# Kernel optimization log

Measured on AMD Instinct MI355X. Metric: run time of the kernel, lower is better.

## Reference

```python
import jax, jax.numpy as jnp
import numpy as np

INPUT_DIM = 768
STATE_DIM = 128
LN_EPS = 1e-5
CLAMP = 10.0


def setup_inputs() -> dict:
    key = jax.random.key(0)
    ks = jax.random.split(key, 9)
    B, T, D, S = 128, 256, INPUT_DIM, STATE_DIM
    x = jax.random.normal(ks[0], (B, T, D), dtype=jnp.float32)
    A = jax.random.normal(ks[1], (S, S), dtype=jnp.float32) * 0.01
    # nn.Linear weights are [out_features, in_features]
    B_w = jax.random.normal(ks[2], (S, D), dtype=jnp.float32) * (1.0 / np.sqrt(D))
    C_w = jax.random.normal(ks[3], (D, S), dtype=jnp.float32) * (1.0 / np.sqrt(S))
    D_w = jax.random.normal(ks[4], (D, D), dtype=jnp.float32) * (1.0 / np.sqrt(D))
    gate_w = jax.random.normal(ks[5], (2, D), dtype=jnp.float32) * (1.0 / np.sqrt(D))
    gate_b = jnp.zeros((2,), dtype=jnp.float32)
    ln_gamma = jnp.ones((D,), dtype=jnp.float32)
    ln_beta = jnp.zeros((D,), dtype=jnp.float32)
    return {"x": x, "A": A, "B_w": B_w, "C_w": C_w, "D_w": D_w,
            "gate_w": gate_w, "gate_b": gate_b,
            "ln_gamma": ln_gamma, "ln_beta": ln_beta}


def reference(x, A, B_w, C_w, D_w, gate_w, gate_b, ln_gamma, ln_beta):
    B, T, D = x.shape
    S = A.shape[0]
    residual = x
    # Precompute input projection for all timesteps: [B, T, S]
    Bx = jnp.einsum('btd,sd->bts', x, B_w)

    def step(state, bx_t):
        # state: [B, S]; state @ A.T + B(x_t), clamped
        state = jnp.clip(state @ A.T + bx_t, -CLAMP, CLAMP)
        return state, state

    init = jnp.zeros((B, S), dtype=x.dtype)
    _, states = jax.lax.scan(step, init, jnp.swapaxes(Bx, 0, 1))  # [T, B, S]
    states = jnp.swapaxes(states, 0, 1)  # [B, T, S]

    # Output projection (vectorized over all timesteps)
    out = jnp.einsum('bts,ds->btd', states, C_w) + jnp.einsum('btd,ed->bte', x, D_w)

    # Gating mix with residual
    gate = jax.nn.softmax(jnp.einsum('btd,gd->btg', x, gate_w) + gate_b, axis=-1)
    out = gate[..., 0:1] * out + gate[..., 1:2] * residual

    # LayerNorm (dropout is identity in eval)
    mu = jnp.mean(out, axis=-1, keepdims=True)
    var = jnp.var(out, axis=-1, keepdims=True)
    out = (out - mu) * jax.lax.rsqrt(var + LN_EPS) * ln_gamma + ln_beta
    return out
```

## Files before the change

kernel.cpp:

```cpp
#include <hip/hip_runtime.h>
#include <hip/hip_bf16.h>
#include <stdint.h>

typedef __bf16 bf16;
typedef __bf16 bf16x4 __attribute__((ext_vector_type(4)));
typedef __bf16 bf16x8 __attribute__((ext_vector_type(8)));
typedef float  f32x4  __attribute__((ext_vector_type(4)));

static constexpr int BB = 128;
static constexpr int TT = 256;
static constexpr int DD = 768;
static constexpr int SS = 128;
static constexpr int MM = BB * TT;
static constexpr int KW1 = DD + SS;

__device__ __forceinline__ void gload16(const void* g, void* l) {
  __builtin_amdgcn_global_load_lds(
      (const __attribute__((address_space(1))) void*)(uintptr_t)g,
      (__attribute__((address_space(3))) void*)(uintptr_t)l, 16, 0, 0);
}

__global__ __launch_bounds__(256) void k0_convert(
    const float* __restrict__ B_w, const float* __restrict__ D_w,
    const float* __restrict__ C_w, bf16* __restrict__ W0, bf16* __restrict__ W1) {
  int i = blockIdx.x * 256 + threadIdx.x;
  if (i < SS * DD) {
    W0[i] = (bf16)B_w[i];
  } else {
    int j = i - SS * DD;
    int n = j / KW1;
    int k = j - n * KW1;
    float v = (k < DD) ? D_w[n * DD + k] : C_w[n * SS + (k - DD)];
    W1[j] = (bf16)v;
  }
}

__global__ __launch_bounds__(256) void k0x_gate(
    const float* __restrict__ x, bf16* __restrict__ xb,
    const float* __restrict__ gw, const float* __restrict__ gb,
    float* __restrict__ glog) {
  const int lane = threadIdx.x & 63;
  const int wv = threadIdx.x >> 6;
  const int r = blockIdx.x * 4 + wv;
  const float4* xr = (const float4*)(x + (size_t)r * DD);
  const float4* g0w = (const float4*)gw;
  const float4* g1w = (const float4*)(gw + DD);
  float d = 0.f;
  #pragma unroll
  for (int i = 0; i < 3; ++i) {
    int c = i * 64 + lane;
    float4 v = xr[c];
    float4 w0 = g0w[c], w1 = g1w[c];
    d += v.x * (w0.x - w1.x) + v.y * (w0.y - w1.y)
       + v.z * (w0.z - w1.z) + v.w * (w0.w - w1.w);
    bf16x4 h;
    h[0] = (bf16)v.x; h[1] = (bf16)v.y; h[2] = (bf16)v.z; h[3] = (bf16)v.w;
    *(bf16x4*)&xb[(size_t)r * DD + c * 4] = h;
  }
  #pragma unroll
  for (int off = 32; off > 0; off >>= 1) d += __shfl_xor(d, off);
  if (lane == 0) glog[r] = d + gb[0] - gb[1];
}

template <int TAG>
__global__ __launch_bounds__(256) void kg(
    const bf16* __restrict__ A1, const bf16* __restrict__ A2,
    const bf16* __restrict__ W, void* __restrict__ Cv,
    int kt1, int kt2, int lda1, int lda2, int ldb, int ldc, int mode) {
  __shared__ __align__(16) bf16 As[128 * 64];
  __shared__ __align__(16) bf16 Bs[128 * 64];

  const int tid = threadIdx.x;
  const int lane = tid & 63;
  const int wv = tid >> 6;
  const int wr = wv >> 1, wc = wv & 1;
  const int lr = lane & 15, lh = lane >> 4;
  const int bn0 = blockIdx.x * 128;
  const int bm0 = blockIdx.y * 128;

  const int l_row = lane >> 3;
  const int l_col = (lane & 7) * 8;

  f32x4 acc[4][4] = {};
  const int KT = kt1 + kt2;

  for (int kt = 0; kt < KT; ++kt) {
    __syncthreads();
    {
      const bf16* Ab; int lda;
      if (kt < kt1) { Ab = A1 + (size_t)bm0 * lda1 + kt * 64; lda = lda1; }
      else          { Ab = A2 + (size_t)bm0 * lda2 + (kt - kt1) * 64; lda = lda2; }
      #pragma unroll
      for (int it = 0; it < 4; ++it) {
        int c = wv * 4 + it;
        gload16(Ab + (size_t)(c * 8 + l_row) * lda + l_col, &As[c * 512]);
      }
    }
    {
      const bf16* Bb = W + (size_t)bn0 * ldb + kt * 64;
      #pragma unroll
      for (int it = 0; it < 4; ++it) {
        int c = wv * 4 + it;
        gload16(Bb + (size_t)(c * 8 + l_row) * ldb + l_col, &Bs[c * 512]);
      }
    }
    __syncthreads();
    #pragma unroll
    for (int kk = 0; kk < 2; ++kk) {
      bf16x8 af[4], bfr[4];
      #pragma unroll
      for (int f = 0; f < 4; ++f)
        af[f] = *(const bf16x8*)&As[(wr * 64 + f * 16 + lr) * 64 + kk * 32 + lh * 8];
      #pragma unroll
      for (int f = 0; f < 4; ++f)
        bfr[f] = *(const bf16x8*)&Bs[(wc * 64 + f * 16 + lr) * 64 + kk * 32 + lh * 8];
      #pragma unroll
      for (int fi = 0; fi < 4; ++fi)
        #pragma unroll
        for (int fj = 0; fj < 4; ++fj)
          acc[fi][fj] = __builtin_amdgcn_mfma_f32_16x16x32_bf16(
              af[fi], bfr[fj], acc[fi][fj], 0, 0, 0);
    }
  }
  #pragma unroll
  for (int fi = 0; fi < 4; ++fi)
    #pragma unroll
    for (int fj = 0; fj < 4; ++fj) {
      int row = bm0 + wr * 64 + fi * 16 + lh * 4;
      int col = bn0 + wc * 64 + fj * 16 + lr;
      if (mode == 0) {
        float* Cp = (float*)Cv + (size_t)row * ldc + col;
        #pragma unroll
        for (int r = 0; r < 4; ++r) Cp[(size_t)r * ldc] = acc[fi][fj][r];
      } else if (mode == 1) {
        bf16* Cp = (bf16*)Cv + (size_t)row * ldc + col;
        #pragma unroll
        for (int r = 0; r < 4; ++r) Cp[(size_t)r * ldc] = (bf16)acc[fi][fj][r];
      } else {
        float* Cp = (float*)Cv + (size_t)row * ldc + col;
        #pragma unroll
        for (int r = 0; r < 4; ++r) Cp[(size_t)r * ldc] += acc[fi][fj][r];
      }
    }
}

__global__ __launch_bounds__(256) void k_fused(
    const bf16* __restrict__ xb, const bf16* __restrict__ W1,
    float* __restrict__ out, bf16* SB, const float* __restrict__ A) {
  __shared__ __align__(16) char sraw[34304];

  if (blockIdx.x < 128) {
    __builtin_amdgcn_s_setprio(1);
    float* st   = (float*)sraw;
    float* part = (float*)(sraw + 1024);
    float* bxb  = (float*)(sraw + 1536);

    const int tid = threadIdx.x;
    const int s = tid & 127;
    const int q = tid >> 7;
    bf16* Bxb = SB + (size_t)blockIdx.x * TT * SS;

    float areg[64];
    {
      const float* Ar = A + s * SS + q * 64;
      #pragma unroll
      for (int j = 0; j < 16; ++j) {
        float4 v = *(const float4*)(Ar + j * 4);
        areg[j * 4 + 0] = v.x; areg[j * 4 + 1] = v.y;
        areg[j * 4 + 2] = v.z; areg[j * 4 + 3] = v.w;
      }
    }
    if (tid < SS) st[tid] = 0.f;

    {
      bf16x8 c0 = *(const bf16x8*)(Bxb + tid * 16);
      bf16x8 c1 = *(const bf16x8*)(Bxb + tid * 16 + 8);
      float* d0 = &bxb[tid * 16];
      #pragma unroll
      for (int e = 0; e < 8; ++e) d0[e] = (float)c0[e];
      #pragma unroll
      for (int e = 0; e < 8; ++e) d0[8 + e] = (float)c1[e];
    }
    bf16x8 n0 = *(const bf16x8*)(Bxb + 4096 + tid * 16);
    bf16x8 n1 = *(const bf16x8*)(Bxb + 4096 + tid * 16 + 8);
    __syncthreads();

    int p = 0, cur = 0;
    for (int ch = 0; ch < 8; ++ch) {
      #pragma unroll 1
      for (int t2 = 0; t2 < 32; ++t2) {
        const float* stp = st + p * SS;
        float a0 = 0.f, a1 = 0.f, a2 = 0.f, a3 = 0.f;
        #pragma unroll
        for (int j = 0; j < 64; j += 4) {
          float4 sv = *(const float4*)(stp + (q << 6) + j);
          a0 += areg[j]     * sv.x;
          a1 += areg[j + 1] * sv.y;
          a2 += areg[j + 2] * sv.z;
          a3 += areg[j + 3] * sv.w;
        }
        float partial = (a0 + a1) + (a2 + a3);
        if (q) part[s] = partial;
        __syncthreads();
        if (!q) {
          float tot = partial + part[s] + bxb[cur * 4096 + t2 * SS + s];
          tot = fminf(10.f, fmaxf(-10.f, tot));
          st[(p ^ 1) * SS + s] = tot;
          Bxb[(size_t)(ch * 32 + t2) * SS + s] = (bf16)tot;
        }
        __syncthreads();
        p ^= 1;
      }
      if (ch < 7) {
        float* dn = &bxb[(cur ^ 1) * 4096 + tid * 16];
        #pragma unroll
        for (int e = 0; e < 8; ++e) dn[e] = (float)n0[e];
        #pragma unroll
        for (int e = 0; e < 8; ++e) dn[8 + e] = (float)n1[e];
        if (ch < 6) {
          n0 = *(const bf16x8*)(Bxb + (ch + 2) * 4096 + tid * 16);
          n1 = *(const bf16x8*)(Bxb + (ch + 2) * 4096 + tid * 16 + 8);
        }
        __syncthreads();
        cur ^= 1;
      }
    }
  } else {
    bf16* As = (bf16*)sraw;
    bf16* Bs = (bf16*)(sraw + 16384);

    const int gb = blockIdx.x - 128;
    const int bn0 = (gb % 6) * 128;
    const int bm0 = (gb / 6) * 128;

    const int tid = threadIdx.x;
    const int lane = tid & 63;
    const int wv = tid >> 6;
    const int wr = wv >> 1, wc = wv & 1;
    const int lr = lane & 15, lh = lane >> 4;
    const int l_row = lane >> 3;
    const int l_col = (lane & 7) * 8;

    f32x4 acc[4][4] = {};

    for (int kt = 0; kt < 12; ++kt) {
      __syncthreads();
      {
        const bf16* Ab = xb + (size_t)bm0 * DD + kt * 64;
        #pragma unroll
        for (int it = 0; it < 4; ++it) {
          int c = wv * 4 + it;
          gload16(Ab + (size_t)(c * 8 + l_row) * DD + l_col, &As[c * 512]);
        }
      }
      {
        const bf16* Bb = W1 + (size_t)bn0 * KW1 + kt * 64;
        #pragma unroll
        for (int it = 0; it < 4; ++it) {
          int c = wv * 4 + it;
          gload16(Bb + (size_t)(c * 8 + l_row) * KW1 + l_col, &Bs[c * 512]);
        }
      }
      __syncthreads();
      #pragma unroll
      for (int kk = 0; kk < 2; ++kk) {
        bf16x8 af[4], bfr[4];
        #pragma unroll
        for (int f = 0; f < 4; ++f)
          af[f] = *(const bf16x8*)&As[(wr * 64 + f * 16 + lr) * 64 + kk * 32 + lh * 8];
        #pragma unroll
        for (int f = 0; f < 4; ++f)
          bfr[f] = *(const bf16x8*)&Bs[(wc * 64 + f * 16 + lr) * 64 + kk * 32 + lh * 8];
        #pragma unroll
        for (int fi = 0; fi < 4; ++fi)
          #pragma unroll
          for (int fj = 0; fj < 4; ++fj)
            acc[fi][fj] = __builtin_amdgcn_mfma_f32_16x16x32_bf16(
                af[fi], bfr[fj], acc[fi][fj], 0, 0, 0);
      }
    }
    #pragma unroll
    for (int fi = 0; fi < 4; ++fi)
      #pragma unroll
      for (int fj = 0; fj < 4; ++fj) {
        int row = bm0 + wr * 64 + fi * 16 + lh * 4;
        int col = bn0 + wc * 64 + fj * 16 + lr;
        float* Cp = out + (size_t)row * DD + col;
        #pragma unroll
        for (int r = 0; r < 4; ++r) Cp[(size_t)r * DD] = acc[fi][fj][r];
      }
  }
}

__global__ __launch_bounds__(256) void kT(
    const bf16* __restrict__ SB, const bf16* __restrict__ Wc,
    float* __restrict__ out, const float* __restrict__ x,
    const float* __restrict__ glog, const float* __restrict__ ln_g,
    const float* __restrict__ ln_b) {
  __shared__ __align__(16) bf16 As[16 * 128];
  __shared__ __align__(16) bf16 Ws[128 * 128];
  __shared__ __align__(16) bf16 mbuf[16 * 768];
  __shared__ float wpart[4][16][2];
  __shared__ float mu_s[16], rs_s[16];

  const int tid = threadIdx.x;
  const int lane = tid & 63;
  const int wv = tid >> 6;
  const int lr = lane & 15, lh = lane >> 4;
  const int m0 = blockIdx.x * 16;

  {
    const bf16* g = SB + (size_t)(m0 + wv * 4 + lh) * 128 + lr * 8;
    gload16(g, &As[wv * 512]);
  }

  float g0v[4], g1v[4];
  #pragma unroll
  for (int r = 0; r < 4; ++r) {
    float gl = glog[m0 + lh * 4 + r];
    float g0 = 1.f / (1.f + expf(-gl));
    g0v[r] = g0; g1v[r] = 1.f - g0;
  }

  float s1[4] = {0.f, 0.f, 0.f, 0.f}, s2[4] = {0.f, 0.f, 0.f, 0.f};

  for (int st = 0; st < 6; ++st) {
    const int n0 = st * 128;
    __syncthreads();
    #pragma unroll
    for (int it = 0; it < 8; ++it) {
      int c = wv * 8 + it;
      const bf16* g = Wc + (size_t)(n0 + c * 4 + lh) * KW1 + lr * 8;
      gload16(g, &Ws[c * 512]);
    }
    __syncthreads();
    f32x4 acc0 = {0.f, 0.f, 0.f, 0.f}, acc1 = {0.f, 0.f, 0.f, 0.f};
    #pragma unroll
    for (int kk = 0; kk < 4; ++kk) {
      bf16x8 af = *(const bf16x8*)&As[lr * 128 + kk * 32 + lh * 8];
      bf16x8 b0 = *(const bf16x8*)&Ws[((wv * 2 + 0) * 16 + lr) * 128 + kk * 32 + lh * 8];
      bf16x8 b1 = *(const bf16x8*)&Ws[((wv * 2 + 1) * 16 + lr) * 128 + kk * 32 + lh * 8];
      acc0 = __builtin_amdgcn_mfma_f32_16x16x32_bf16(af, b0, acc0, 0, 0, 0);
      acc1 = __builtin_amdgcn_mfma_f32_16x16x32_bf16(af, b1, acc1, 0, 0, 0);
    }
    #pragma unroll
    for (int nn = 0; nn < 2; ++nn) {
      const f32x4 av = nn ? acc1 : acc0;
      int col = n0 + (wv * 2 + nn) * 16 + lr;
      #pragma unroll
      for (int r = 0; r < 4; ++r) {
        int rowl = lh * 4 + r;
        size_t gi = (size_t)(m0 + rowl) * DD + col;
        float raw = av[r] + out[gi];
        float mv = g0v[r] * raw + g1v[r] * x[gi];
        s1[r] += mv; s2[r] += mv * mv;
        mbuf[rowl * DD + col] = (bf16)mv;
      }
    }
  }
  #pragma unroll
  for (int r = 0; r < 4; ++r) {
    #pragma unroll
    for (int off = 1; off < 16; off <<= 1) {
      s1[r] += __shfl_xor(s1[r], off);
      s2[r] += __shfl_xor(s2[r], off);
    }
  }
  if (lr == 0) {
    #pragma unroll
    for (int r = 0; r < 4; ++r) {
      wpart[wv][lh * 4 + r][0] = s1[r];
      wpart[wv][lh * 4 + r][1] = s2[r];
    }
  }
  __syncthreads();
  if (tid < 16) {
    float S1 = wpart[0][tid][0] + wpart[1][tid][0] + wpart[2][tid][0] + wpart[3][tid][0];
    float S2 = wpart[0][tid][1] + wpart[1][tid][1] + wpart[2][tid][1] + wpart[3][tid][1];
    float mu = S1 * (1.f / 768.f);
    float var = S2 * (1.f / 768.f) - mu * mu;
    mu_s[tid] = mu;
    rs_s[tid] = rsqrtf(fmaxf(var, 0.f) + 1e-5f);
  }
  __syncthreads();
  #pragma unroll
  for (int i = 0; i < 12; ++i) {
    int gq = i * 256 + tid;
    int row = gq / 192;
    int c4 = gq - row * 192;
    int col = c4 * 4;
    bf16x4 mv = *(const bf16x4*)&mbuf[row * DD + col];
    float4 gg = *(const float4*)&ln_g[col];
    float4 bb = *(const float4*)&ln_b[col];
    float mu = mu_s[row], rs = rs_s[row];
    float4 y;
    y.x = ((float)mv[0] - mu) * rs * gg.x + bb.x;
    y.y = ((float)mv[1] - mu) * rs * gg.y + bb.y;
    y.z = ((float)mv[2] - mu) * rs * gg.z + bb.z;
    y.w = ((float)mv[3] - mu) * rs * gg.w + bb.w;
    *(float4*)&out[(size_t)(m0 + row) * DD + col] = y;
  }
}

__global__ __launch_bounds__(256) void k_gemm(
    const float* __restrict__ A1, const bf16* __restrict__ A2,
    const bf16* __restrict__ W, float* __restrict__ C,
    int kt1, int kt2, int lda1, int lda2, int ldb, int ldc) {
  __shared__ __align__(16) bf16 As[128][72];
  __shared__ __align__(16) bf16 Bs[128][72];

  const int tid = threadIdx.x;
  const int lane = tid & 63;
  const int wv = tid >> 6;
  const int wr = wv >> 1, wc = wv & 1;
  const int lr = lane & 15, lh = lane >> 4;
  const int bn0 = blockIdx.x * 128;
  const int bm0 = blockIdx.y * 128;

  f32x4 acc[4][4] = {};
  const int KT = kt1 + kt2;

  for (int kt = 0; kt < KT; ++kt) {
    __syncthreads();
    if (kt < kt1) {
      const float* Ab = A1 + (size_t)bm0 * lda1 + kt * 64;
      #pragma unroll
      for (int it = 0; it < 8; ++it) {
        int c = it * 256 + tid;
        int row = c >> 4, col = (c & 15) << 2;
        float4 v = *(const float4*)(Ab + (size_t)row * lda1 + col);
        bf16x4 h;
        h[0] = (bf16)v.x; h[1] = (bf16)v.y; h[2] = (bf16)v.z; h[3] = (bf16)v.w;
        *(bf16x4*)&As[row][col] = h;
      }
    } else {
      const bf16* Ab = A2 + (size_t)bm0 * lda2 + (kt - kt1) * 64;
      #pragma unroll
      for (int it = 0; it < 8; ++it) {
        int c = it * 256 + tid;
        int row = c >> 4, col = (c & 15) << 2;
        bf16x4 v = *(const bf16x4*)(Ab + (size_t)row * lda2 + col);
        *(bf16x4*)&As[row][col] = v;
      }
    }
    {
      const bf16* Bb = W + (size_t)bn0 * ldb + kt * 64;
      #pragma unroll
      for (int it = 0; it < 8; ++it) {
        int c = it * 256 + tid;
        int row = c >> 4, col = (c & 15) << 2;
        bf16x4 v = *(const bf16x4*)(Bb + (size_t)row * ldb + col);
        *(bf16x4*)&Bs[row][col] = v;
      }
    }
    __syncthreads();
    #pragma unroll
    for (int kk = 0; kk < 2; ++kk) {
      bf16x8 af[4], bfr[4];
      #pragma unroll
      for (int f = 0; f < 4; ++f)
        af[f] = *(const bf16x8*)&As[wr * 64 + f * 16 + lr][kk * 32 + lh * 8];
      #pragma unroll
      for (int f = 0; f < 4; ++f)
        bfr[f] = *(const bf16x8*)&Bs[wc * 64 + f * 16 + lr][kk * 32 + lh * 8];
      #pragma unroll
      for (int fi = 0; fi < 4; ++fi)
        #pragma unroll
        for (int fj = 0; fj < 4; ++fj)
          acc[fi][fj] = __builtin_amdgcn_mfma_f32_16x16x32_bf16(
              af[fi], bfr[fj], acc[fi][fj], 0, 0, 0);
    }
  }
  #pragma unroll
  for (int fi = 0; fi < 4; ++fi)
    #pragma unroll
    for (int fj = 0; fj < 4; ++fj) {
      int row = bm0 + wr * 64 + fi * 16 + lh * 4;
      int col = bn0 + wc * 64 + fj * 16 + lr;
      float* Cp = C + (size_t)row * ldc + col;
      #pragma unroll
      for (int r = 0; r < 4; ++r) Cp[(size_t)r * ldc] = acc[fi][fj][r];
    }
}

__global__ __launch_bounds__(512) void k2_scan(
    const float* __restrict__ Bx, const float* __restrict__ A,
    bf16* __restrict__ states) {
  __shared__ __align__(16) float st[2][SS];
  __shared__ __align__(16) float part[3][SS];
  __shared__ __align__(16) float bxb[2][32 * SS];

  const int tid = threadIdx.x;
  const int s = tid & 127;
  const int q = tid >> 7;
  const int b = blockIdx.x;

  float areg[32];
  {
    const float* Ar = A + s * SS + q * 32;
    #pragma unroll
    for (int j = 0; j < 8; ++j) {
      float4 v = *(const float4*)(Ar + j * 4);
      areg[j * 4 + 0] = v.x; areg[j * 4 + 1] = v.y;
      areg[j * 4 + 2] = v.z; areg[j * 4 + 3] = v.w;
    }
  }
  if (tid < SS) st[0][tid] = 0.f;

  const float* Bxb = Bx + (size_t)b * TT * SS;
  {
    float4 c0 = *(const float4*)(Bxb + tid * 4);
    float4 c1 = *(const float4*)(Bxb + 2048 + tid * 4);
    *(float4*)&bxb[0][tid * 4] = c0;
    *(float4*)&bxb[0][2048 + tid * 4] = c1;
  }
  float4 n0 = *(const float4*)(Bxb + 4096 + tid * 4);
  float4 n1 = *(const float4*)(Bxb + 4096 + 2048 + tid * 4);
  __syncthreads();

  bf16* so = states + (size_t)b * TT * SS;
  int p = 0, cur = 0;
  for (int ch = 0; ch < 8; ++ch) {
    #pragma unroll 1
    for (int t2 = 0; t2 < 32; ++t2) {
      const float* stp = st[p];
      float a0 = 0.f, a1 = 0.f, a2 = 0.f, a3 = 0.f;
      #pragma unroll
      for (int j = 0; j < 32; j += 4) {
        float4 sv = *(const float4*)(stp + (q << 5) + j);
        a0 += areg[j]     * sv.x;
        a1 += areg[j + 1] * sv.y;
        a2 += areg[j + 2] * sv.z;
        a3 += areg[j + 3] * sv.w;
      }
      float partial = (a0 + a1) + (a2 + a3);
      if (q) part[q - 1][s] = partial;
      __syncthreads();
      if (q == 0) {
        float tot = partial + part[0][s] + part[1][s] + part[2][s]
                  + bxb[cur][t2 * SS + s];
        tot = fminf(10.f, fmaxf(-10.f, tot));
        st[p ^ 1][s] = tot;
        so[(size_t)(ch * 32 + t2) * SS + s] = (bf16)tot;
      }
      __syncthreads();
      p ^= 1;
    }
    if (ch < 7) {
      *(float4*)&bxb[cur ^ 1][tid * 4] = n0;
      *(float4*)&bxb[cur ^ 1][2048 + tid * 4] = n1;
      if (ch < 6) {
        n0 = *(const float4*)(Bxb + (ch + 2) * 4096 + tid * 4);
        n1 = *(const float4*)(Bxb + (ch + 2) * 4096 + 2048 + tid * 4);
      }
      __syncthreads();
      cur ^= 1;
    }
  }
}

__global__ __launch_bounds__(256) void k4_epilogue(
    float* __restrict__ out, const float* __restrict__ x,
    const float* __restrict__ gate_w, const float* __restrict__ gate_b,
    const float* __restrict__ ln_g, const float* __restrict__ ln_b) {
  const int lane = threadIdx.x & 63;
  const int w = threadIdx.x >> 6;
  const int r = blockIdx.x * 4 + w;

  float4* orow = (float4*)(out + (size_t)r * DD);
  const float4* xrow = (const float4*)(x + (size_t)r * DD);
  const float4* g0w = (const float4*)gate_w;
  const float4* g1w = (const float4*)(gate_w + DD);

  float4 o[3], xv[3];
  float d = 0.f;
  #pragma unroll
  for (int i = 0; i < 3; ++i) {
    int c = i * 64 + lane;
    o[i] = orow[c];
    xv[i] = xrow[c];
    float4 w0 = g0w[c], w1 = g1w[c];
    d += xv[i].x * (w0.x - w1.x) + xv[i].y * (w0.y - w1.y)
       + xv[i].z * (w0.z - w1.z) + xv[i].w * (w0.w - w1.w);
  }
  #pragma unroll
  for (int off = 32; off > 0; off >>= 1) d += __shfl_xor(d, off);
  d += gate_b[0] - gate_b[1];
  float g0 = 1.f / (1.f + expf(-d));
  float g1 = 1.f - g0;

  float4 m[3];
  float s1 = 0.f, s2 = 0.f;
  #pragma unroll
  for (int i = 0; i < 3; ++i) {
    m[i].x = g0 * o[i].x + g1 * xv[i].x;
    m[i].y = g0 * o[i].y + g1 * xv[i].y;
    m[i].z = g0 * o[i].z + g1 * xv[i].z;
    m[i].w = g0 * o[i].w + g1 * xv[i].w;
    s1 += (m[i].x + m[i].y) + (m[i].z + m[i].w);
    s2 += (m[i].x * m[i].x + m[i].y * m[i].y)
        + (m[i].z * m[i].z + m[i].w * m[i].w);
  }
  #pragma unroll
  for (int off = 32; off > 0; off >>= 1) {
    s1 += __shfl_xor(s1, off);
    s2 += __shfl_xor(s2, off);
  }
  float mu = s1 * (1.f / 768.f);
  float var = s2 * (1.f / 768.f) - mu * mu;
  float rs = rsqrtf(var + 1e-5f);

  #pragma unroll
  for (int i = 0; i < 3; ++i) {
    int c = i * 64 + lane;
    float4 gg = ((const float4*)ln_g)[c];
    float4 bb = ((const float4*)ln_b)[c];
    float4 y;
    y.x = (m[i].x - mu) * rs * gg.x + bb.x;
    y.y = (m[i].y - mu) * rs * gg.y + bb.y;
    y.z = (m[i].z - mu) * rs * gg.z + bb.z;
    y.w = (m[i].w - mu) * rs * gg.w + bb.w;
    orow[c] = y;
  }
}

extern "C" void kernel_launch(void* const* d_in, const int* in_sizes, int n_in,
                              void* d_out, int out_size, void* d_ws, size_t ws_size,
                              hipStream_t stream) {
  const float* x   = (const float*)d_in[0];
  const float* A   = (const float*)d_in[1];
  const float* B_w = (const float*)d_in[2];
  const float* C_w = (const float*)d_in[3];
  const float* D_w = (const float*)d_in[4];
  const float* gw  = (const float*)d_in[5];
  const float* gb  = (const float*)d_in[6];
  const float* lng = (const float*)d_in[7];
  const float* lnb = (const float*)d_in[8];
  float* out = (float*)d_out;

  bf16* W0 = (bf16*)d_ws;
  bf16* W1 = W0 + SS * DD;
  bf16* SB = W1 + DD * KW1;
  bf16* xb = SB + (size_t)MM * SS;
  float* glog = (float*)(xb + (size_t)MM * DD);
  const size_t base_bf16 =
      2ull * (SS * DD + DD * KW1 + (size_t)MM * SS + (size_t)MM * DD);
  const size_t ws_need_full = base_bf16 + 4ull * MM;
  const size_t ws_need_min = 2ull * (SS * DD + DD * KW1 + (size_t)MM * SS);

  k0_convert<<<dim3(3072), dim3(256), 0, stream>>>(B_w, D_w, C_w, W0, W1);

  if (ws_size >= ws_need_full) {
    k0x_gate<<<dim3(8192), dim3(256), 0, stream>>>(x, xb, gw, gb, glog);
    kg<1><<<dim3(1, 256), dim3(256), 0, stream>>>(
        xb, nullptr, W0, SB, 12, 0, DD, 0, DD, SS, 1);
    k_fused<<<dim3(128 + 1536), dim3(256), 0, stream>>>(xb, W1, out, SB, A);
    kT<<<dim3(2048), dim3(256), 0, stream>>>(
        SB, W1 + DD, out, x, glog, lng, lnb);
  } else if (ws_size >= ws_need_min) {
    float* Bx = out + ((size_t)MM * DD - (size_t)MM * SS);
    bf16* states = SB;
    k_gemm<<<dim3(1, 256), dim3(256), 0, stream>>>(
        x, nullptr, W0, Bx, 12, 0, DD, 0, DD, SS);
    k2_scan<<<dim3(128), dim3(512), 0, stream>>>(Bx, A, states);
    k_gemm<<<dim3(6, 256), dim3(256), 0, stream>>>(
        x, states, W1, out, 12, 2, DD, SS, KW1, DD);
    k4_epilogue<<<dim3(8192), dim3(256), 0, stream>>>(out, x, gw, gb, lng, lnb);
  }
}
```

Measured before the change: 411.3 us.

## Swizzle LDS tiles, widen fused GEMM blocks to 512 threads, split scan four ways

Applies an XOR swizzle to the LDS layouts of the GEMM tiles in kg, k_fused and kT, so that the MFMA fragment reads avoid bank conflicts. The fused kernel moves to 512-thread blocks. Its GEMM part now computes 128x256 tiles with 8 waves over half as many blocks, which improves reuse of the A tile. The scan part splits the 128-wide dot product across four thread groups, each holding 32 A values in registers, and keeps the Bx chunk in LDS as bf16 instead of converting it to fp32. The cost is a three-way partial-sum reduction on every step, plus more LDS and threads per block, which may lower occupancy for the GEMM blocks running alongside the scan.

```diff
diff --git a/kernel.cpp b/kernel.cpp
--- a/kernel.cpp
+++ b/kernel.cpp
@@ -79,7 +79,7 @@
   const int bm0 = blockIdx.y * 128;
 
   const int l_row = lane >> 3;
-  const int l_col = (lane & 7) * 8;
+  const int l_col = ((lane & 7) ^ l_row) * 8;
 
   f32x4 acc[4][4] = {};
   const int KT = kt1 + kt2;
@@ -107,13 +107,14 @@
     __syncthreads();
     #pragma unroll
     for (int kk = 0; kk < 2; ++kk) {
+      const int ec = (kk * 32 + lh * 8) ^ ((lr & 7) * 8);
       bf16x8 af[4], bfr[4];
       #pragma unroll
       for (int f = 0; f < 4; ++f)
-        af[f] = *(const bf16x8*)&As[(wr * 64 + f * 16 + lr) * 64 + kk * 32 + lh * 8];
+        af[f] = *(const bf16x8*)&As[(wr * 64 + f * 16 + lr) * 64 + ec];
       #pragma unroll
       for (int f = 0; f < 4; ++f)
-        bfr[f] = *(const bf16x8*)&Bs[(wc * 64 + f * 16 + lr) * 64 + kk * 32 + lh * 8];
+        bfr[f] = *(const bf16x8*)&Bs[(wc * 64 + f * 16 + lr) * 64 + ec];
       #pragma unroll
       for (int fi = 0; fi < 4; ++fi)
         #pragma unroll
@@ -144,27 +145,27 @@
     }
 }
 
-__global__ __launch_bounds__(256) void k_fused(
+__global__ __launch_bounds__(512) void k_fused(
     const bf16* __restrict__ xb, const bf16* __restrict__ W1,
     float* __restrict__ out, bf16* SB, const float* __restrict__ A) {
-  __shared__ __align__(16) char sraw[34304];
+  __shared__ __align__(16) char sraw[49152];
 
   if (blockIdx.x < 128) {
     __builtin_amdgcn_s_setprio(1);
     float* st   = (float*)sraw;
     float* part = (float*)(sraw + 1024);
-    float* bxb  = (float*)(sraw + 1536);
+    bf16* bxbB  = (bf16*)(sraw + 2560);
 
     const int tid = threadIdx.x;
     const int s = tid & 127;
     const int q = tid >> 7;
     bf16* Bxb = SB + (size_t)blockIdx.x * TT * SS;
 
-    float areg[64];
+    float areg[32];
     {
-      const float* Ar = A + s * SS + q * 64;
-      #pragma unroll
-      for (int j = 0; j < 16; ++j) {
+      const float* Ar = A + s * SS + q * 32;
+      #pragma unroll
+      for (int j = 0; j < 8; ++j) {
         float4 v = *(const float4*)(Ar + j * 4);
         areg[j * 4 + 0] = v.x; areg[j * 4 + 1] = v.y;
         areg[j * 4 + 2] = v.z; areg[j * 4 + 3] = v.w;
@@ -172,17 +173,8 @@
     }
     if (tid < SS) st[tid] = 0.f;
 
-    {
-      bf16x8 c0 = *(const bf16x8*)(Bxb + tid * 16);
-      bf16x8 c1 = *(const bf16x8*)(Bxb + tid * 16 + 8);
-      float* d0 = &bxb[tid * 16];
-      #pragma unroll
-      for (int e = 0; e < 8; ++e) d0[e] = (float)c0[e];
-      #pragma unroll
-      for (int e = 0; e < 8; ++e) d0[8 + e] = (float)c1[e];
-    }
-    bf16x8 n0 = *(const bf16x8*)(Bxb + 4096 + tid * 16);
-    bf16x8 n1 = *(const bf16x8*)(Bxb + 4096 + tid * 16 + 8);
+    *(bf16x8*)&bxbB[tid * 8] = *(const bf16x8*)(Bxb + tid * 8);
+    bf16x8 nx = *(const bf16x8*)(Bxb + 4096 + tid * 8);
     __syncthreads();
 
     int p = 0, cur = 0;
@@ -192,18 +184,19 @@
         const float* stp = st + p * SS;
         float a0 = 0.f, a1 = 0.f, a2 = 0.f, a3 = 0.f;
         #pragma unroll
-        for (int j = 0; j < 64; j += 4) {
-          float4 sv = *(const float4*)(stp + (q << 6) + j);
+        for (int j = 0; j < 32; j += 4) {
+          float4 sv = *(const float4*)(stp + (q << 5) + j);
           a0 += areg[j]     * sv.x;
           a1 += areg[j + 1] * sv.y;
           a2 += areg[j + 2] * sv.z;
           a3 += areg[j + 3] * sv.w;
         }
         float partial = (a0 + a1) + (a2 + a3);
-        if (q) part[s] = partial;
+        if (q) part[(q - 1) * SS + s] = partial;
         __syncthreads();
-        if (!q) {
-          float tot = partial + part[s] + bxb[cur * 4096 + t2 * SS + s];
+        if (q == 0) {
+          float tot = partial + part[s] + part[SS + s] + part[2 * SS + s]
+                    + (float)bxbB[cur * 4096 + t2 * SS + s];
           tot = fminf(10.f, fmaxf(-10.f, tot));
           st[(p ^ 1) * SS + s] = tot;
           Bxb[(size_t)(ch * 32 + t2) * SS + s] = (bf16)tot;
@@ -212,15 +205,8 @@
         p ^= 1;
       }
       if (ch < 7) {
-        float* dn = &bxb[(cur ^ 1) * 4096 + tid * 16];
-        #pragma unroll
-        for (int e = 0; e < 8; ++e) dn[e] = (float)n0[e];
-        #pragma unroll
-        for (int e = 0; e < 8; ++e) dn[8 + e] = (float)n1[e];
-        if (ch < 6) {
-          n0 = *(const bf16x8*)(Bxb + (ch + 2) * 4096 + tid * 16);
-          n1 = *(const bf16x8*)(Bxb + (ch + 2) * 4096 + tid * 16 + 8);
-        }
+        *(bf16x8*)&bxbB[(cur ^ 1) * 4096 + tid * 8] = nx;
+        if (ch < 6) nx = *(const bf16x8*)(Bxb + (ch + 2) * 4096 + tid * 8);
         __syncthreads();
         cur ^= 1;
       }
@@ -230,16 +216,16 @@
     bf16* Bs = (bf16*)(sraw + 16384);
 
     const int gb = blockIdx.x - 128;
-    const int bn0 = (gb % 6) * 128;
-    const int bm0 = (gb / 6) * 128;
+    const int bm0 = (gb / 3) * 128;
+    const int bn0 = (gb % 3) * 256;
 
     const int tid = threadIdx.x;
     const int lane = tid & 63;
     const int wv = tid >> 6;
-    const int wr = wv >> 1, wc = wv & 1;
+    const int wr = wv >> 2, wc = wv & 3;
     const int lr = lane & 15, lh = lane >> 4;
     const int l_row = lane >> 3;
-    const int l_col = (lane & 7) * 8;
+    const int l_col = ((lane & 7) ^ l_row) * 8;
 
     f32x4 acc[4][4] = {};
 
@@ -248,8 +234,8 @@
       {
         const bf16* Ab = xb + (size_t)bm0 * DD + kt * 64;
         #pragma unroll
-        for (int it = 0; it < 4; ++it) {
-          int c = wv * 4 + it;
+        for (int it = 0; it < 2; ++it) {
+          int c = wv * 2 + it;
           gload16(Ab + (size_t)(c * 8 + l_row) * DD + l_col, &As[c * 512]);
         }
       }
@@ -264,13 +250,14 @@
       __syncthreads();
       #pragma unroll
       for (int kk = 0; kk < 2; ++kk) {
+        const int ec = (kk * 32 + lh * 8) ^ ((lr & 7) * 8);
         bf16x8 af[4], bfr[4];
         #pragma unroll
         for (int f = 0; f < 4; ++f)
-          af[f] = *(const bf16x8*)&As[(wr * 64 + f * 16 + lr) * 64 + kk * 32 + lh * 8];
+          af[f] = *(const bf16x8*)&As[(wr * 64 + f * 16 + lr) * 64 + ec];
         #pragma unroll
         for (int f = 0; f < 4; ++f)
-          bfr[f] = *(const bf16x8*)&Bs[(wc * 64 + f * 16 + lr) * 64 + kk * 32 + lh * 8];
+          bfr[f] = *(const bf16x8*)&Bs[(wc * 64 + f * 16 + lr) * 64 + ec];
         #pragma unroll
         for (int fi = 0; fi < 4; ++fi)
           #pragma unroll
@@ -310,7 +297,8 @@
   const int m0 = blockIdx.x * 16;
 
   {
-    const bf16* g = SB + (size_t)(m0 + wv * 4 + lh) * 128 + lr * 8;
+    const int r7 = (wv * 4 + lh) & 7;
+    const bf16* g = SB + (size_t)(m0 + wv * 4 + lh) * 128 + ((lr ^ r7) * 8);
     gload16(g, &As[wv * 512]);
   }
 
@@ -330,16 +318,18 @@
     #pragma unroll
     for (int it = 0; it < 8; ++it) {
       int c = wv * 8 + it;
-      const bf16* g = Wc + (size_t)(n0 + c * 4 + lh) * KW1 + lr * 8;
+      const int r7 = (c * 4 + lh) & 7;
+      const bf16* g = Wc + (size_t)(n0 + c * 4 + lh) * KW1 + ((lr ^ r7) * 8);
       gload16(g, &Ws[c * 512]);
     }
     __syncthreads();
     f32x4 acc0 = {0.f, 0.f, 0.f, 0.f}, acc1 = {0.f, 0.f, 0.f, 0.f};
     #pragma unroll
     for (int kk = 0; kk < 4; ++kk) {
-      bf16x8 af = *(const bf16x8*)&As[lr * 128 + kk * 32 + lh * 8];
-      bf16x8 b0 = *(const bf16x8*)&Ws[((wv * 2 + 0) * 16 + lr) * 128 + kk * 32 + lh * 8];
-      bf16x8 b1 = *(const bf16x8*)&Ws[((wv * 2 + 1) * 16 + lr) * 128 + kk * 32 + lh * 8];
+      const int ec = (kk * 32 + lh * 8) ^ ((lr & 7) * 8);
+      bf16x8 af = *(const bf16x8*)&As[lr * 128 + ec];
+      bf16x8 b0 = *(const bf16x8*)&Ws[((wv * 2 + 0) * 16 + lr) * 128 + ec];
+      bf16x8 b1 = *(const bf16x8*)&Ws[((wv * 2 + 1) * 16 + lr) * 128 + ec];
       acc0 = __builtin_amdgcn_mfma_f32_16x16x32_bf16(af, b0, acc0, 0, 0, 0);
       acc1 = __builtin_amdgcn_mfma_f32_16x16x32_bf16(af, b1, acc1, 0, 0, 0);
     }
@@ -654,7 +644,7 @@
     k0x_gate<<<dim3(8192), dim3(256), 0, stream>>>(x, xb, gw, gb, glog);
     kg<1><<<dim3(1, 256), dim3(256), 0, stream>>>(
         xb, nullptr, W0, SB, 12, 0, DD, 0, DD, SS, 1);
-    k_fused<<<dim3(128 + 1536), dim3(256), 0, stream>>>(xb, W1, out, SB, A);
+    k_fused<<<dim3(128 + 768), dim3(512), 0, stream>>>(xb, W1, out, SB, A);
     kT<<<dim3(2048), dim3(256), 0, stream>>>(
         SB, W1 + DD, out, x, glog, lng, lnb);
   } else if (ws_size >= ws_need_min) {
```

Result: faster. 358.8 us (-12.8%).
